# Kernel tuning notes

Measured on AMD Instinct MI355X. Metric: run time of the kernel, lower is better.

Reference implementation:

```python
import jax, jax.numpy as jnp
import numpy as np

DIM = 768
NUM_HEADS = 12
HEAD_DIM = DIM // NUM_HEADS  # 64
IMG_W = 32
IMG_H = 32
B = 16
N = IMG_W * IMG_H + 1  # 1025 (CLS + grid)


def setup_inputs() -> dict:
    key = jax.random.key(0)
    k1, k2, k3, k4, k5 = jax.random.split(key, 5)
    x = jax.random.normal(k1, (B, N, DIM), dtype=jnp.float32)
    W_qkv = jax.random.normal(k2, (3 * DIM, DIM), dtype=jnp.float32) * 0.02
    W_proj = jax.random.normal(k3, (DIM, DIM), dtype=jnp.float32) * 0.02
    b_proj = jax.random.normal(k4, (DIM,), dtype=jnp.float32) * 0.02
    # learned mixed-RoPE frequencies, shape (2, num_heads * head_dim//2)
    freqs = jax.random.normal(k5, (2, NUM_HEADS * (HEAD_DIM // 2)), dtype=jnp.float32) * 0.1
    return {"x": x, "W_qkv": W_qkv, "W_proj": W_proj, "b_proj": b_proj, "freqs": freqs}


def _mixed_angles(freqs):
    # t_x = t % W, t_y = t // W over the flattened grid (init_t_xy)
    t = jnp.arange(IMG_W * IMG_H, dtype=jnp.float32)
    t_x = t % IMG_W
    t_y = jnp.floor(t / IMG_W)
    # outer products -> (N-1, H, hd/2) -> (H, N-1, hd/2); angle = fx + fy
    fx = (t_x[:, None] * freqs[0][None, :]).reshape(-1, NUM_HEADS, HEAD_DIM // 2)
    fy = (t_y[:, None] * freqs[1][None, :]).reshape(-1, NUM_HEADS, HEAD_DIM // 2)
    return (fx + fy).transpose(1, 0, 2)  # (H, N-1, hd/2)


def _apply_rope(t, cos, sin):
    # t: (B, H, N-1, hd); complex multiply on (even, odd) pairs
    pairs = t.reshape(*t.shape[:-1], HEAD_DIM // 2, 2)
    x0, x1 = pairs[..., 0], pairs[..., 1]
    o0 = x0 * cos - x1 * sin
    o1 = x0 * sin + x1 * cos
    return jnp.stack([o0, o1], axis=-1).reshape(t.shape)


def reference(x, W_qkv, W_proj, b_proj, freqs):
    Bx, Nx, C = x.shape
    scale = HEAD_DIM ** -0.5
    qkv = jnp.einsum('bnc,dc->bnd', x, W_qkv)  # Linear, no bias
    qkv = qkv.reshape(Bx, Nx, 3, NUM_HEADS, HEAD_DIM).transpose(2, 0, 3, 1, 4)
    q, k, v = qkv[0], qkv[1], qkv[2]  # (B, H, N, hd)

    ang = _mixed_angles(freqs)  # (H, N-1, hd/2)
    cos, sin = jnp.cos(ang), jnp.sin(ang)  # broadcast over batch

    # rotate all tokens except the leading CLS token
    q = jnp.concatenate([q[:, :, :1], _apply_rope(q[:, :, 1:], cos, sin)], axis=2)
    k = jnp.concatenate([k[:, :, :1], _apply_rope(k[:, :, 1:], cos, sin)], axis=2)

    attn = jax.nn.softmax(jnp.einsum('bhqd,bhkd->bhqk', q * scale, k), axis=-1)
    out = jnp.einsum('bhqk,bhkd->bhqd', attn, v)  # (B, H, N, hd)
    out = out.transpose(0, 2, 1, 3).reshape(Bx, Nx, C)
    return out @ W_proj.T + b_proj
```

## Files before the change

kernel.cpp:

```cpp
#include <hip/hip_runtime.h>
#include <math.h>

#define DIM     768
#define NH      12
#define HD      64
#define NTOK    1025
#define BATCH   16
#define MTOT    (BATCH * NTOK)
#define QKVD    (3 * DIM)

typedef short  short8 __attribute__((ext_vector_type(8)));
typedef float  f32x4  __attribute__((ext_vector_type(4)));

typedef const __attribute__((address_space(1))) void gvoid_t;
typedef __attribute__((address_space(3)))       void lvoid_t;
#define GLD16(gsrc, ldst) __builtin_amdgcn_global_load_lds( \
    (gvoid_t*)(gsrc), (lvoid_t*)(ldst), 16, 0, 0)

static __device__ __forceinline__ unsigned int f2bf(float f) {
    unsigned int u = __float_as_uint(f);
    u += 0x7FFFu + ((u >> 16) & 1u);
    return u >> 16;
}

__device__ __forceinline__ void cvt8(const float* __restrict__ src,
                                     unsigned short* __restrict__ dst, int i) {
    float4 a = *(const float4*)(src + (size_t)i*8);
    float4 b = *(const float4*)(src + (size_t)i*8 + 4);
    uint4 pk;
    pk.x = f2bf(a.x) | (f2bf(a.y) << 16);
    pk.y = f2bf(a.z) | (f2bf(a.w) << 16);
    pk.z = f2bf(b.x) | (f2bf(b.y) << 16);
    pk.w = f2bf(b.z) | (f2bf(b.w) << 16);
    *(uint4*)(dst + (size_t)i*8) = pk;
}

__global__ __launch_bounds__(256) void cvt_bf16_kernel(
    const float* __restrict__ x, const float* __restrict__ Wq,
    const float* __restrict__ Wp,
    unsigned short* __restrict__ xb, unsigned short* __restrict__ Wqb,
    unsigned short* __restrict__ Wpb)
{
    const int stride = gridDim.x * blockDim.x;
    const int tid = blockIdx.x * blockDim.x + threadIdx.x;
    for (int i = tid; i < MTOT*DIM/8;  i += stride) cvt8(x,  xb,  i);
    for (int i = tid; i < QKVD*DIM/8;  i += stride) cvt8(Wq, Wqb, i);
    for (int i = tid; i < DIM*DIM/8;   i += stride) cvt8(Wp, Wpb, i);
}

__global__ __launch_bounds__(256) void rope_tab_kernel(
    const float* __restrict__ freqs, float2* __restrict__ tab)
{
    const int gid = blockIdx.x * 256 + threadIdx.x;
    const int p  = gid & 31;
    const int n1 = (gid >> 5) & 1023;
    const int h  = gid >> 15;
    const float tx = (float)(n1 & 31), ty = (float)(n1 >> 5);
    const float ang = tx * freqs[h*32 + p] + ty * freqs[384 + h*32 + p];
    float s, c;
    sincosf(ang, &s, &c);
    tab[gid] = make_float2(c, s);
}

__device__ __forceinline__ void gemm_core(
    const unsigned short* __restrict__ Wb,
    const unsigned short* __restrict__ Xb,
    int D0, int T0, int maxXrow,
    short* Ws, short* Xs, f32x4 acc[4][4], int tid)
{
    const int lane = tid & 63;
    const int wu   = __builtin_amdgcn_readfirstlane(tid >> 6);
    const int wr   = wu >> 1, wc = wu & 1;
    const int l4   = lane >> 4, l15 = lane & 15;

    const int srow = lane >> 3;
    const int schk = (lane & 7) ^ srow;
    const unsigned short* wsrc[4];
    const unsigned short* xsrc[4];
#pragma unroll
    for (int i = 0; i < 4; ++i) {
        int r = wu*32 + i*8 + srow;
        wsrc[i] = Wb + (size_t)(D0 + r) * DIM + schk*8;
        int xr = T0 + r; if (xr > maxXrow) xr = maxXrow;
        xsrc[i] = Xb + (size_t)xr * DIM + schk*8;
    }

    for (int kt = 0; kt < DIM/64; ++kt) {
        __syncthreads();
#pragma unroll
        for (int i = 0; i < 4; ++i) {
            GLD16(wsrc[i] + kt*64, &Ws[(wu*4 + i) * 512]);
            GLD16(xsrc[i] + kt*64, &Xs[(wu*4 + i) * 512]);
        }
        __syncthreads();

        short8 wf[4][2], xf[4][2];
#pragma unroll
        for (int f = 0; f < 4; ++f) {
            const int rw = wr*64 + f*16 + l15;
            const int rx = wc*64 + f*16 + l15;
#pragma unroll
            for (int kf = 0; kf < 2; ++kf) {
                wf[f][kf] = *(const short8*)&Ws[rw*64 + (((kf*4 + l4) ^ (rw & 7)) << 3)];
                xf[f][kf] = *(const short8*)&Xs[rx*64 + (((kf*4 + l4) ^ (rx & 7)) << 3)];
            }
        }
        __builtin_amdgcn_s_setprio(1);
#pragma unroll
        for (int kf = 0; kf < 2; ++kf)
#pragma unroll
            for (int fm = 0; fm < 4; ++fm)
#pragma unroll
                for (int fn = 0; fn < 4; ++fn)
                    acc[fm][fn] = __builtin_amdgcn_mfma_f32_16x16x32_bf16(
                        wf[fm][kf], xf[fn][kf], acc[fm][fn], 0, 0, 0);
        __builtin_amdgcn_s_setprio(0);
    }
}

__global__ __launch_bounds__(256) void qkv_gemm_kernel(
    const unsigned short* __restrict__ Wqb, const unsigned short* __restrict__ xb,
    const float2* __restrict__ tab,
    unsigned short* __restrict__ Qb, unsigned short* __restrict__ Kb,
    unsigned short* __restrict__ Vb)
{
    __shared__ __align__(16) short Ws[128*64];
    __shared__ __align__(16) short Xs[128*64];
    f32x4 acc[4][4] = {};
    const int tid = threadIdx.x;
    const int D0 = blockIdx.x * 128;
    const int T0 = blockIdx.y * 128;
    gemm_core(Wqb, xb, D0, T0, MTOT - 1, Ws, Xs, acc, tid);

    const int lane = tid & 63;
    const int wu = tid >> 6, wr = wu >> 1, wc = wu & 1;
    const int l4 = lane >> 4, l15 = lane & 15;
    const int which = D0 / DIM;
    unsigned short* dst = (which == 0) ? Qb : (which == 1) ? Kb : Vb;

    unsigned bArr[4], nArr[4];
    bool vArr[4];
#pragma unroll
    for (int fn = 0; fn < 4; ++fn) {
        unsigned m = T0 + wc*64 + fn*16 + l15;
        vArr[fn] = m < MTOT;
        bArr[fn] = m / NTOK;
        nArr[fn] = m - bArr[fn]*NTOK;
    }
#pragma unroll
    for (int fm = 0; fm < 4; ++fm) {
        const int hcol = (D0 % DIM) + wr*64 + fm*16 + l4*4;
        const int h = hcol >> 6, dd = hcol & 63;
        const int p0 = dd >> 1;
#pragma unroll
        for (int fn = 0; fn < 4; ++fn) {
            if (!vArr[fn]) continue;
            f32x4 a = acc[fm][fn];
            const int n = nArr[fn];
            if (which < 2) {
                int n1 = n > 0 ? n - 1 : 0;
                float4 cs = *(const float4*)&tab[(size_t)(h*1024 + n1)*32 + p0];
                if (n == 0) cs = make_float4(1.f, 0.f, 1.f, 0.f);
                float e0 = a[0], od0 = a[1], e1 = a[2], od1 = a[3];
                a[0] = e0*cs.x - od0*cs.y;  a[1] = e0*cs.y + od0*cs.x;
                a[2] = e1*cs.z - od1*cs.w;  a[3] = e1*cs.w + od1*cs.z;
            }
            uint2 pk;
            pk.x = f2bf(a[0]) | (f2bf(a[1]) << 16);
            pk.y = f2bf(a[2]) | (f2bf(a[3]) << 16);
            *(uint2*)&dst[((size_t)(bArr[fn]*NH + h)*NTOK + n)*HD + dd] = pk;
        }
    }
}

__global__ __launch_bounds__(256) void attn_mfma_kernel(
    const unsigned short* __restrict__ Qb,
    const unsigned short* __restrict__ Kb,
    const unsigned short* __restrict__ Vb,
    unsigned short* __restrict__ Obf)
{
    __shared__ __align__(16) char KsR[2][8192];
    __shared__ __align__(16) char VtR[2][8192];
    __shared__ __align__(16) char PsR[4][4096];

    const int tid  = threadIdx.x;
    const int lane = tid & 63;
    const int w    = __builtin_amdgcn_readfirstlane(tid >> 6);
    const int l4   = lane >> 4, l15 = lane & 15, l7 = lane & 7;

    const int d    = blockIdx.x;
    const int xcd  = d & 7;
    const int s    = d >> 3;
    const int bh   = xcd * 24 + s / 9;
    const int q0   = (s % 9) * 128;
    const size_t base = (size_t)bh * NTOK * HD;
    const float C = 0.125f * 1.44269504089f;

    short8 qf[2][2];
#pragma unroll
    for (int qg = 0; qg < 2; ++qg) {
        int qr = q0 + w*32 + qg*16 + l15;
        int qrc = qr < NTOK ? qr : NTOK - 1;
        qf[qg][0] = *(const short8*)(Qb + base + (size_t)qrc*HD + l4*8);
        qf[qg][1] = *(const short8*)(Qb + base + (size_t)qrc*HD + 32 + l4*8);
    }

    float mA = -INFINITY, mB = -INFINITY, lA = 0.f, lB = 0.f;
    f32x4 oA[4] = {}, oB[4] = {};

    const int ktokb = tid >> 3;
    const int kchk  = tid & 7;
    const int vtok  = ((tid & 7) << 3) | ((tid >> 3) & 7);
    const int vc    = vtok >> 3;
    const int vb2   = (vtok & 7) * 2;
    char* Pw = &PsR[w][0];

#pragma unroll
    for (int i = 0; i < 2; ++i) {
        int tok = ktokb + i*32;
        int gk = tok; if (gk > NTOK-1) gk = NTOK-1;
        int sc = kchk ^ (tok & 7);
        GLD16(Kb + base + (size_t)gk*HD + sc*8, &KsR[0][w*1024 + i*4096]);
    }
    uint4 vg[2];
#pragma unroll
    for (int i = 0; i < 2; ++i) {
        int gv = vtok;
        vg[i] = (gv < NTOK)
            ? *(const uint4*)(Vb + base + (size_t)gv*HD + w*8 + i*32)
            : make_uint4(0,0,0,0);
    }

    for (int kt = 0; kt < 17; ++kt) {
        const int buf = kt & 1;

#pragma unroll
        for (int i = 0; i < 2; ++i) {
            const int vd0 = w*8 + i*32;
            unsigned short vs[8];
            vs[0]=(unsigned short)vg[i].x; vs[1]=(unsigned short)(vg[i].x>>16);
            vs[2]=(unsigned short)vg[i].y; vs[3]=(unsigned short)(vg[i].y>>16);
            vs[4]=(unsigned short)vg[i].z; vs[5]=(unsigned short)(vg[i].z>>16);
            vs[6]=(unsigned short)vg[i].w; vs[7]=(unsigned short)(vg[i].w>>16);
#pragma unroll
            for (int j = 0; j < 8; ++j)
                *(unsigned short*)(&VtR[buf][0] + (vd0+j)*128 + ((vc ^ j) << 4) + vb2) = vs[j];
        }
        __syncthreads();

        {
            const int ktn = (kt + 1 < 17) ? kt + 1 : 16;
            const int nb  = buf ^ 1;
#pragma unroll
            for (int i = 0; i < 2; ++i) {
                int tok = ktokb + i*32;
                int gk = ktn*64 + tok; if (gk > NTOK-1) gk = NTOK-1;
                int sc = kchk ^ (tok & 7);
                GLD16(Kb + base + (size_t)gk*HD + sc*8, &KsR[nb][w*1024 + i*4096]);
            }
#pragma unroll
            for (int i = 0; i < 2; ++i) {
                int gv = ktn*64 + vtok;
                vg[i] = (gv < NTOK)
                    ? *(const uint4*)(Vb + base + (size_t)gv*HD + w*8 + i*32)
                    : make_uint4(0,0,0,0);
            }
        }

        f32x4 sA[4] = {}, sB[4] = {};
        __builtin_amdgcn_s_setprio(1);
#pragma unroll
        for (int tg = 0; tg < 4; ++tg) {
            const int row = tg*16 + l15;
            short8 ka0 = *(const short8*)(&KsR[buf][0] + row*128 + ((l4 ^ l7) << 4));
            short8 ka1 = *(const short8*)(&KsR[buf][0] + row*128 + (((4 + l4) ^ l7) << 4));
            sA[tg] = __builtin_amdgcn_mfma_f32_16x16x32_bf16(ka0, qf[0][0], sA[tg], 0,0,0);
            sA[tg] = __builtin_amdgcn_mfma_f32_16x16x32_bf16(ka1, qf[0][1], sA[tg], 0,0,0);
            sB[tg] = __builtin_amdgcn_mfma_f32_16x16x32_bf16(ka0, qf[1][0], sB[tg], 0,0,0);
            sB[tg] = __builtin_amdgcn_mfma_f32_16x16x32_bf16(ka1, qf[1][1], sB[tg], 0,0,0);
        }
        __builtin_amdgcn_s_setprio(0);

        float pA[16], pB[16];
#pragma unroll
        for (int tg = 0; tg < 4; ++tg)
#pragma unroll
            for (int r = 0; r < 4; ++r) { pA[tg*4+r] = sA[tg][r]; pB[tg*4+r] = sB[tg][r]; }

        if (kt == 16) {
#pragma unroll
            for (int i = 0; i < 16; ++i) {
                int tok = 1024 + (i>>2)*16 + l4*4 + (i&3);
                if (tok > 1024) { pA[i] = -3e38f; pB[i] = -3e38f; }
            }
        }

        float mlA = pA[0], mlB = pB[0];
#pragma unroll
        for (int i = 1; i < 16; ++i) { mlA = fmaxf(mlA, pA[i]); mlB = fmaxf(mlB, pB[i]); }
        mlA = fmaxf(mlA, __shfl_xor(mlA, 16)); mlA = fmaxf(mlA, __shfl_xor(mlA, 32));
        mlB = fmaxf(mlB, __shfl_xor(mlB, 16)); mlB = fmaxf(mlB, __shfl_xor(mlB, 32));

        bool grow = (mlA > mA + 32.f) || (mlB > mB + 32.f);
        if (__any(grow)) {
            float mnA = fmaxf(mA, mlA), mnB = fmaxf(mB, mlB);
            float alA = __builtin_exp2f((mA - mnA) * C);
            float alB = __builtin_exp2f((mB - mnB) * C);
            mA = mnA; mB = mnB;
            lA *= alA; lB *= alB;
            f32x4 arA, arB;
#pragma unroll
            for (int r = 0; r < 4; ++r) {
                arA[r] = __shfl(alA, l4*4 + r);
                arB[r] = __shfl(alB, l4*4 + r);
            }
#pragma unroll
            for (int dg = 0; dg < 4; ++dg) { oA[dg] *= arA; oB[dg] *= arB; }
        }

        const float mcA = mA * C, mcB = mB * C;
        float psA = 0.f, psB = 0.f;
#pragma unroll
        for (int i = 0; i < 16; ++i) {
            pA[i] = __builtin_exp2f(pA[i]*C - mcA); psA += pA[i];
            pB[i] = __builtin_exp2f(pB[i]*C - mcB); psB += pB[i];
        }
        psA += __shfl_xor(psA, 16); psA += __shfl_xor(psA, 32);
        psB += __shfl_xor(psB, 16); psB += __shfl_xor(psB, 32);
        lA += psA; lB += psB;

#pragma unroll
        for (int tg = 0; tg < 4; ++tg) {
            unsigned k0a, k1a, k0b, k1b;
            asm volatile("v_cvt_pk_bf16_f32 %0, %1, %2" : "=v"(k0a) : "v"(pA[tg*4+0]), "v"(pA[tg*4+1]));
            asm volatile("v_cvt_pk_bf16_f32 %0, %1, %2" : "=v"(k1a) : "v"(pA[tg*4+2]), "v"(pA[tg*4+3]));
            asm volatile("v_cvt_pk_bf16_f32 %0, %1, %2" : "=v"(k0b) : "v"(pB[tg*4+0]), "v"(pB[tg*4+1]));
            asm volatile("v_cvt_pk_bf16_f32 %0, %1, %2" : "=v"(k1b) : "v"(pB[tg*4+2]), "v"(pB[tg*4+3]));
            const int chk = (((tg*2 + (l4 >> 1)) ^ l7) << 4) + (l4 & 1)*8;
            *(uint2*)(Pw + l15*128      + chk) = make_uint2(k0a, k1a);
            *(uint2*)(Pw + (16+l15)*128 + chk) = make_uint2(k0b, k1b);
        }
        __builtin_amdgcn_wave_barrier();

        const short8 pf00 = *(const short8*)(Pw + l15*128      + ((l4 ^ l7) << 4));
        const short8 pf01 = *(const short8*)(Pw + l15*128      + (((4+l4) ^ l7) << 4));
        const short8 pf10 = *(const short8*)(Pw + (16+l15)*128 + ((l4 ^ l7) << 4));
        const short8 pf11 = *(const short8*)(Pw + (16+l15)*128 + (((4+l4) ^ l7) << 4));

        __builtin_amdgcn_s_setprio(1);
#pragma unroll
        for (int dg = 0; dg < 4; ++dg) {
            const int dd = dg*16 + l15;
            short8 v0 = *(const short8*)(&VtR[buf][0] + dd*128 + ((l4 ^ (dd & 7)) << 4));
            short8 v1 = *(const short8*)(&VtR[buf][0] + dd*128 + (((4 + l4) ^ (dd & 7)) << 4));
            oA[dg] = __builtin_amdgcn_mfma_f32_16x16x32_bf16(pf00, v0, oA[dg], 0,0,0);
            oA[dg] = __builtin_amdgcn_mfma_f32_16x16x32_bf16(pf01, v1, oA[dg], 0,0,0);
            oB[dg] = __builtin_amdgcn_mfma_f32_16x16x32_bf16(pf10, v0, oB[dg], 0,0,0);
            oB[dg] = __builtin_amdgcn_mfma_f32_16x16x32_bf16(pf11, v1, oB[dg], 0,0,0);
        }
        __builtin_amdgcn_s_setprio(0);
        __syncthreads();
    }

    const float liA = 1.f / lA, liB = 1.f / lB;
    f32x4 lvA, lvB;
#pragma unroll
    for (int r = 0; r < 4; ++r) {
        lvA[r] = __shfl(liA, l4*4 + r);
        lvB[r] = __shfl(liB, l4*4 + r);
    }
    const int b = bh / NH, h = bh % NH;
#pragma unroll
    for (int dg = 0; dg < 4; ++dg)
#pragma unroll
        for (int r = 0; r < 4; ++r) {
            int rowA = q0 + w*32 + l4*4 + r;
            int rowB = rowA + 16;
            if (rowA < NTOK)
                Obf[((size_t)b*NTOK + rowA)*DIM + h*HD + dg*16 + l15] =
                    (unsigned short)f2bf(oA[dg][r] * lvA[r]);
            if (rowB < NTOK)
                Obf[((size_t)b*NTOK + rowB)*DIM + h*HD + dg*16 + l15] =
                    (unsigned short)f2bf(oB[dg][r] * lvB[r]);
        }
}

__global__ __launch_bounds__(256) void proj_gemm_kernel(
    const unsigned short* __restrict__ Wpb, const unsigned short* __restrict__ Obf,
    const float* __restrict__ bp, float* __restrict__ out)
{
    __shared__ __align__(16) short Ws[128*64];
    __shared__ __align__(16) short Xs[128*64];
    f32x4 acc[4][4] = {};
    const int tid = threadIdx.x;
    const int D0 = blockIdx.x * 128;
    const int T0 = blockIdx.y * 128;
    gemm_core(Wpb, Obf, D0, T0, MTOT - 1, Ws, Xs, acc, tid);

    const int lane = tid & 63;
    const int wu = tid >> 6, wr = wu >> 1, wc = wu & 1;
    const int l4 = lane >> 4, l15 = lane & 15;

    unsigned mArr[4];
    bool vArr[4];
#pragma unroll
    for (int fn = 0; fn < 4; ++fn) {
        unsigned m = T0 + wc*64 + fn*16 + l15;
        mArr[fn] = m;
        vArr[fn] = m < MTOT;
    }
#pragma unroll
    for (int fm = 0; fm < 4; ++fm) {
        const int nG = D0 + wr*64 + fm*16 + l4*4;
        const float4 bias = *(const float4*)&bp[nG];
#pragma unroll
        for (int fn = 0; fn < 4; ++fn) {
            if (!vArr[fn]) continue;
            f32x4 a = acc[fm][fn];
            float4 v = make_float4(a[0]+bias.x, a[1]+bias.y, a[2]+bias.z, a[3]+bias.w);
            *(float4*)&out[(size_t)mArr[fn]*DIM + nG] = v;
        }
    }
}

extern "C" void kernel_launch(void* const* d_in, const int* in_sizes, int n_in,
                              void* d_out, int out_size, void* d_ws, size_t ws_size,
                              hipStream_t stream)
{
    const float* x     = (const float*)d_in[0];
    const float* Wqkv  = (const float*)d_in[1];
    const float* Wp    = (const float*)d_in[2];
    const float* bp    = (const float*)d_in[3];
    const float* freqs = (const float*)d_in[4];
    float* out = (float*)d_out;

    const size_t SZ = (size_t)BATCH * NH * NTOK * HD;
    unsigned short* Qb  = (unsigned short*)d_ws;
    unsigned short* Kb  = Qb + SZ;
    unsigned short* Vb  = Kb + SZ;
    unsigned short* Obf = Vb + SZ;
    unsigned short* xb  = Obf + SZ;
    unsigned short* Wqb = xb + SZ;
    unsigned short* Wpb = Wqb + (size_t)QKVD * DIM;
    float2*         tab = (float2*)(Wpb + (size_t)DIM * DIM);

    cvt_bf16_kernel<<<2048, 256, 0, stream>>>(x, Wqkv, Wp, xb, Wqb, Wpb);
    rope_tab_kernel<<<1536, 256, 0, stream>>>(freqs, tab);
    qkv_gemm_kernel<<<dim3(QKVD/128, (MTOT + 127)/128), 256, 0, stream>>>(
        Wqb, xb, tab, Qb, Kb, Vb);
    attn_mfma_kernel<<<1728, 256, 0, stream>>>(Qb, Kb, Vb, Obf);
    proj_gemm_kernel<<<dim3(DIM/128, (MTOT + 127)/128), 256, 0, stream>>>(
        Wpb, Obf, bp, out);
}
```

Before: 326.9 us.

## Transpose PV MFMA operands, prefetch V one tile ahead, drop trailing barrier

Swaps the operand order of the P·V MFMAs so the output accumulator is laid out with query rows along lanes. This removes the per-row shuffles for the rescale factor and the final normalizer, and lets each lane write packed 4-element bf16 stores to the output. The V tile is now written into the next LDS buffer one iteration early, with the register prefetch moved two tiles ahead, so the second __syncthreads per iteration can be removed. The ordering between LDS writes to the other buffer and reads of the current one now rests on a single barrier, which narrows the margin for race errors.

```diff
diff --git a/kernel.cpp b/kernel.cpp
--- a/kernel.cpp
+++ b/kernel.cpp
@@ -21,6 +21,17 @@
     unsigned int u = __float_as_uint(f);
     u += 0x7FFFu + ((u >> 16) & 1u);
     return u >> 16;
+}
+
+static __device__ __forceinline__ float red_max(float x) {
+    x = fmaxf(x, __shfl_xor(x, 16));
+    x = fmaxf(x, __shfl_xor(x, 32));
+    return x;
+}
+static __device__ __forceinline__ float red_sum(float x) {
+    x += __shfl_xor(x, 16);
+    x += __shfl_xor(x, 32);
+    return x;
 }
 
 __device__ __forceinline__ void cvt8(const float* __restrict__ src,
@@ -215,17 +226,31 @@
     const int vb2   = (vtok & 7) * 2;
     char* Pw = &PsR[w][0];
 
+    uint4 vg[2];
+#pragma unroll
+    for (int i = 0; i < 2; ++i)
+        vg[i] = *(const uint4*)(Vb + base + (size_t)vtok*HD + w*8 + i*32);
 #pragma unroll
     for (int i = 0; i < 2; ++i) {
         int tok = ktokb + i*32;
-        int gk = tok; if (gk > NTOK-1) gk = NTOK-1;
         int sc = kchk ^ (tok & 7);
-        GLD16(Kb + base + (size_t)gk*HD + sc*8, &KsR[0][w*1024 + i*4096]);
-    }
-    uint4 vg[2];
+        GLD16(Kb + base + (size_t)tok*HD + sc*8, &KsR[0][w*1024 + i*4096]);
+    }
 #pragma unroll
     for (int i = 0; i < 2; ++i) {
-        int gv = vtok;
+        const int vd0 = w*8 + i*32;
+        unsigned short vs[8];
+        vs[0]=(unsigned short)vg[i].x; vs[1]=(unsigned short)(vg[i].x>>16);
+        vs[2]=(unsigned short)vg[i].y; vs[3]=(unsigned short)(vg[i].y>>16);
+        vs[4]=(unsigned short)vg[i].z; vs[5]=(unsigned short)(vg[i].z>>16);
+        vs[6]=(unsigned short)vg[i].w; vs[7]=(unsigned short)(vg[i].w>>16);
+#pragma unroll
+        for (int j = 0; j < 8; ++j)
+            *(unsigned short*)(&VtR[0][0] + (vd0+j)*128 + ((vc ^ j) << 4) + vb2) = vs[j];
+    }
+#pragma unroll
+    for (int i = 0; i < 2; ++i) {
+        int gv = 64 + vtok;
         vg[i] = (gv < NTOK)
             ? *(const uint4*)(Vb + base + (size_t)gv*HD + w*8 + i*32)
             : make_uint4(0,0,0,0);
@@ -233,31 +258,30 @@
 
     for (int kt = 0; kt < 17; ++kt) {
         const int buf = kt & 1;
-
-#pragma unroll
-        for (int i = 0; i < 2; ++i) {
-            const int vd0 = w*8 + i*32;
-            unsigned short vs[8];
-            vs[0]=(unsigned short)vg[i].x; vs[1]=(unsigned short)(vg[i].x>>16);
-            vs[2]=(unsigned short)vg[i].y; vs[3]=(unsigned short)(vg[i].y>>16);
-            vs[4]=(unsigned short)vg[i].z; vs[5]=(unsigned short)(vg[i].z>>16);
-            vs[6]=(unsigned short)vg[i].w; vs[7]=(unsigned short)(vg[i].w>>16);
-#pragma unroll
-            for (int j = 0; j < 8; ++j)
-                *(unsigned short*)(&VtR[buf][0] + (vd0+j)*128 + ((vc ^ j) << 4) + vb2) = vs[j];
-        }
         __syncthreads();
 
-        {
-            const int ktn = (kt + 1 < 17) ? kt + 1 : 16;
-            const int nb  = buf ^ 1;
+        if (kt < 16) {
+            const int nb = buf ^ 1;
 #pragma unroll
             for (int i = 0; i < 2; ++i) {
                 int tok = ktokb + i*32;
-                int gk = ktn*64 + tok; if (gk > NTOK-1) gk = NTOK-1;
+                int gk = (kt+1)*64 + tok; if (gk > NTOK-1) gk = NTOK-1;
                 int sc = kchk ^ (tok & 7);
                 GLD16(Kb + base + (size_t)gk*HD + sc*8, &KsR[nb][w*1024 + i*4096]);
             }
+#pragma unroll
+            for (int i = 0; i < 2; ++i) {
+                const int vd0 = w*8 + i*32;
+                unsigned short vs[8];
+                vs[0]=(unsigned short)vg[i].x; vs[1]=(unsigned short)(vg[i].x>>16);
+                vs[2]=(unsigned short)vg[i].y; vs[3]=(unsigned short)(vg[i].y>>16);
+                vs[4]=(unsigned short)vg[i].z; vs[5]=(unsigned short)(vg[i].z>>16);
+                vs[6]=(unsigned short)vg[i].w; vs[7]=(unsigned short)(vg[i].w>>16);
+#pragma unroll
+                for (int j = 0; j < 8; ++j)
+                    *(unsigned short*)(&VtR[nb][0] + (vd0+j)*128 + ((vc ^ j) << 4) + vb2) = vs[j];
+            }
+            const int ktn = (kt+2 < 17) ? kt+2 : 16;
 #pragma unroll
             for (int i = 0; i < 2; ++i) {
                 int gv = ktn*64 + vtok;
@@ -298,8 +322,8 @@
         float mlA = pA[0], mlB = pB[0];
 #pragma unroll
         for (int i = 1; i < 16; ++i) { mlA = fmaxf(mlA, pA[i]); mlB = fmaxf(mlB, pB[i]); }
-        mlA = fmaxf(mlA, __shfl_xor(mlA, 16)); mlA = fmaxf(mlA, __shfl_xor(mlA, 32));
-        mlB = fmaxf(mlB, __shfl_xor(mlB, 16)); mlB = fmaxf(mlB, __shfl_xor(mlB, 32));
+        mlA = red_max(mlA);
+        mlB = red_max(mlB);
 
         bool grow = (mlA > mA + 32.f) || (mlB > mB + 32.f);
         if (__any(grow)) {
@@ -308,14 +332,8 @@
             float alB = __builtin_exp2f((mB - mnB) * C);
             mA = mnA; mB = mnB;
             lA *= alA; lB *= alB;
-            f32x4 arA, arB;
-#pragma unroll
-            for (int r = 0; r < 4; ++r) {
-                arA[r] = __shfl(alA, l4*4 + r);
-                arB[r] = __shfl(alB, l4*4 + r);
-            }
-#pragma unroll
-            for (int dg = 0; dg < 4; ++dg) { oA[dg] *= arA; oB[dg] *= arB; }
+#pragma unroll
+            for (int dg = 0; dg < 4; ++dg) { oA[dg] *= alA; oB[dg] *= alB; }
         }
 
         const float mcA = mA * C, mcB = mB * C;
@@ -325,9 +343,8 @@
             pA[i] = __builtin_exp2f(pA[i]*C - mcA); psA += pA[i];
             pB[i] = __builtin_exp2f(pB[i]*C - mcB); psB += pB[i];
         }
-        psA += __shfl_xor(psA, 16); psA += __shfl_xor(psA, 32);
-        psB += __shfl_xor(psB, 16); psB += __shfl_xor(psB, 32);
-        lA += psA; lB += psB;
+        lA += red_sum(psA);
+        lB += red_sum(psB);
 
 #pragma unroll
         for (int tg = 0; tg < 4; ++tg) {
@@ -353,36 +370,38 @@
             const int dd = dg*16 + l15;
             short8 v0 = *(const short8*)(&VtR[buf][0] + dd*128 + ((l4 ^ (dd & 7)) << 4));
             short8 v1 = *(const short8*)(&VtR[buf][0] + dd*128 + (((4 + l4) ^ (dd & 7)) << 4));
-            oA[dg] = __builtin_amdgcn_mfma_f32_16x16x32_bf16(pf00, v0, oA[dg], 0,0,0);
-            oA[dg] = __builtin_amdgcn_mfma_f32_16x16x32_bf16(pf01, v1, oA[dg], 0,0,0);
-            oB[dg] = __builtin_amdgcn_mfma_f32_16x16x32_bf16(pf10, v0, oB[dg], 0,0,0);
-            oB[dg] = __builtin_amdgcn_mfma_f32_16x16x32_bf16(pf11, v1, oB[dg], 0,0,0);
+            oA[dg] = __builtin_amdgcn_mfma_f32_16x16x32_bf16(v0, pf00, oA[dg], 0,0,0);
+            oA[dg] = __builtin_amdgcn_mfma_f32_16x16x32_bf16(v1, pf01, oA[dg], 0,0,0);
+            oB[dg] = __builtin_amdgcn_mfma_f32_16x16x32_bf16(v0, pf10, oB[dg], 0,0,0);
+            oB[dg] = __builtin_amdgcn_mfma_f32_16x16x32_bf16(v1, pf11, oB[dg], 0,0,0);
         }
         __builtin_amdgcn_s_setprio(0);
-        __syncthreads();
     }
 
     const float liA = 1.f / lA, liB = 1.f / lB;
-    f32x4 lvA, lvB;
-#pragma unroll
-    for (int r = 0; r < 4; ++r) {
-        lvA[r] = __shfl(liA, l4*4 + r);
-        lvB[r] = __shfl(liB, l4*4 + r);
-    }
     const int b = bh / NH, h = bh % NH;
-#pragma unroll
-    for (int dg = 0; dg < 4; ++dg)
-#pragma unroll
-        for (int r = 0; r < 4; ++r) {
-            int rowA = q0 + w*32 + l4*4 + r;
-            int rowB = rowA + 16;
-            if (rowA < NTOK)
-                Obf[((size_t)b*NTOK + rowA)*DIM + h*HD + dg*16 + l15] =
-                    (unsigned short)f2bf(oA[dg][r] * lvA[r]);
-            if (rowB < NTOK)
-                Obf[((size_t)b*NTOK + rowB)*DIM + h*HD + dg*16 + l15] =
-                    (unsigned short)f2bf(oB[dg][r] * lvB[r]);
-        }
+    const int qA = q0 + w*32 + l15;
+    const int qB = qA + 16;
+    if (qA < NTOK) {
+        unsigned short* p = Obf + ((size_t)b*NTOK + qA)*DIM + h*HD + l4*4;
+#pragma unroll
+        for (int dg = 0; dg < 4; ++dg) {
+            uint2 pk;
+            pk.x = f2bf(oA[dg][0]*liA) | (f2bf(oA[dg][1]*liA) << 16);
+            pk.y = f2bf(oA[dg][2]*liA) | (f2bf(oA[dg][3]*liA) << 16);
+            *(uint2*)(p + dg*16) = pk;
+        }
+    }
+    if (qB < NTOK) {
+        unsigned short* p = Obf + ((size_t)b*NTOK + qB)*DIM + h*HD + l4*4;
+#pragma unroll
+        for (int dg = 0; dg < 4; ++dg) {
+            uint2 pk;
+            pk.x = f2bf(oB[dg][0]*liB) | (f2bf(oB[dg][1]*liB) << 16);
+            pk.y = f2bf(oB[dg][2]*liB) | (f2bf(oB[dg][3]*liB) << 16);
+            *(uint2*)(p + dg*16) = pk;
+        }
+    }
 }
 
 __global__ __launch_bounds__(256) void proj_gemm_kernel(
```

Measured after the change: 318.8 us. 2.5% less time.
